# Kernel tuning notes

Hardware: AMD Instinct MI355X
Metric: run time of the kernel (lower is better)

The kernel has to match this reference:

```python
import jax, jax.numpy as jnp
import numpy as np

HEADS = 8
DIM_HEAD = 64
EPS = 1e-5  # PyTorch InstanceNorm default eps


def _instance_norm_lastdim(t):
    # PyTorch InstanceNorm1d on (b*h, n, d) with affine=False normalizes over
    # the last (spatial) axis d per (sample, token), biased variance.
    mu = jnp.mean(t, axis=-1, keepdims=True)
    var = jnp.mean(jnp.square(t - mu), axis=-1, keepdims=True)
    return (t - mu) / jnp.sqrt(var + EPS)


def setup_inputs() -> dict:
    key = jax.random.key(0)
    k1, k2, k3, k4, k5 = jax.random.split(key, 5)
    b, n1, n2, dim = 4, 8192, 8192, 256
    inner = HEADS * DIM_HEAD  # 512
    return {
        "x": jax.random.normal(k1, (b, n1, dim), jnp.float32),
        "z": jax.random.normal(k2, (b, n2, dim), jnp.float32),
        "Wq": jax.random.normal(k3, (dim, inner), jnp.float32) * 0.02,
        "Wkv": jax.random.normal(k4, (dim, 2 * inner), jnp.float32) * 0.02,
        "Wout": jax.random.normal(k5, (inner, dim), jnp.float32) * 0.02,
        "bout": jnp.zeros((dim,), jnp.float32),
    }


def reference(x, z, Wq, Wkv, Wout, bout):
    b, n1, _ = x.shape
    n2 = z.shape[1]
    h, d = HEADS, DIM_HEAD

    q = x @ Wq                     # [b, n1, h*d]
    kv = z @ Wkv                   # [b, n2, 2*h*d]
    k, v = jnp.split(kv, 2, axis=-1)

    q = q.reshape(b, n1, h, d).transpose(0, 2, 1, 3)  # b h n1 d
    k = k.reshape(b, n2, h, d).transpose(0, 2, 1, 3)  # b h n2 d
    v = v.reshape(b, n2, h, d).transpose(0, 2, 1, 3)  # b h n2 d

    # galerkin: normalize k and v
    k = _instance_norm_lastdim(k)
    v = _instance_norm_lastdim(v)

    # linear-attention kernel trick: (k^T v) then q @ dots, scaled by 1/n2
    dots = jnp.einsum('bhnd,bhne->bhde', k, v)          # [b, h, d, d]
    out = jnp.einsum('bhnd,bhde->bhne', q, dots) / n2   # [b, h, n1, d]

    out = out.transpose(0, 2, 1, 3).reshape(b, n1, h * d)
    return out @ Wout + bout
```

## Files before the change

### kernel.cpp

```cpp
#include <hip/hip_runtime.h>
#include <cstddef>

#define NB    4
#define NTOK  8192
#define DIMX  256
#define NH    8
#define HD    64
#define INNER 512
#define SPLIT 16
#define EPS   1e-5f

typedef __attribute__((ext_vector_type(8))) short short8;
typedef __attribute__((ext_vector_type(4))) float f32x4;

__device__ __forceinline__ unsigned short f2bf(float f) {
  union { float f; unsigned u; } v; v.f = f;
  unsigned r = v.u + 0x7fffu + ((v.u >> 16) & 1u);
  return (unsigned short)(r >> 16);
}

__global__ __launch_bounds__(256) void k_pre(
    const float* __restrict__ z, unsigned short* __restrict__ zb,
    const float* __restrict__ Wkv, unsigned short* __restrict__ wkvT)
{
  __shared__ unsigned short t[64][68];
  if (blockIdx.x < 2048) {
    const size_t i = ((size_t)blockIdx.x * 256 + threadIdx.x) * 16;
    float4 a0 = *(const float4*)(z + i);
    float4 a1 = *(const float4*)(z + i + 4);
    float4 a2 = *(const float4*)(z + i + 8);
    float4 a3 = *(const float4*)(z + i + 12);
    short8 p0, p1;
    p0[0] = (short)f2bf(a0.x); p0[1] = (short)f2bf(a0.y);
    p0[2] = (short)f2bf(a0.z); p0[3] = (short)f2bf(a0.w);
    p0[4] = (short)f2bf(a1.x); p0[5] = (short)f2bf(a1.y);
    p0[6] = (short)f2bf(a1.z); p0[7] = (short)f2bf(a1.w);
    p1[0] = (short)f2bf(a2.x); p1[1] = (short)f2bf(a2.y);
    p1[2] = (short)f2bf(a2.z); p1[3] = (short)f2bf(a2.w);
    p1[4] = (short)f2bf(a3.x); p1[5] = (short)f2bf(a3.y);
    p1[6] = (short)f2bf(a3.z); p1[7] = (short)f2bf(a3.w);
    *(short8*)(zb + i) = p0;
    *(short8*)(zb + i + 8) = p1;
  } else {
    const int tid = threadIdx.x;
    const int bb = blockIdx.x - 2048;
    const int r0 = (bb & 3) * 64;
    const int c0 = (bb >> 2) * 64;
    const int r = tid >> 2;
    const int c4 = (tid & 3) * 16;
#pragma unroll
    for (int j = 0; j < 4; ++j) {
      float4 v = *(const float4*)(Wkv + (size_t)(r0 + r) * (2 * INNER) + c0 + c4 + j * 4);
      t[r][c4 + j * 4 + 0] = f2bf(v.x);
      t[r][c4 + j * 4 + 1] = f2bf(v.y);
      t[r][c4 + j * 4 + 2] = f2bf(v.z);
      t[r][c4 + j * 4 + 3] = f2bf(v.w);
    }
    __syncthreads();
    const int cc = tid >> 2;
    const int rr4 = (tid & 3) * 16;
    short8 o0, o1;
#pragma unroll
    for (int i = 0; i < 8; ++i) o0[i] = (short)t[rr4 + i][cc];
#pragma unroll
    for (int i = 0; i < 8; ++i) o1[i] = (short)t[rr4 + 8 + i][cc];
    unsigned short* dst = wkvT + (size_t)(c0 + cc) * DIMX + r0 + rr4;
    *(short8*)(dst) = o0;
    *(short8*)(dst + 8) = o1;
  }
}

__global__ __launch_bounds__(256) void k_dots_mfma(
    const unsigned short* __restrict__ zb, const unsigned short* __restrict__ wkvT,
    float* __restrict__ partial)
{
  const int tid  = threadIdx.x;
  const int lane = tid & 63;
  const int w    = tid >> 6;
  const int l15  = lane & 15;
  const int lg   = lane >> 4;

  const int bid = blockIdx.x;
  const int s = bid & (SPLIT - 1);
  const int h = (bid >> 4) & (NH - 1);
  const int b = bid >> 7;

  __shared__ unsigned short zs[32][268];
  __shared__ unsigned short kv2[128][36];
  __shared__ float sum1[4][32];
  __shared__ float sum2[4][32];

  short8 awf[2][8];
#pragma unroll
  for (int mf = 0; mf < 2; ++mf) {
    const int dim = w * 32 + mf * 16 + l15;
    const int gd = (dim < HD) ? (h * HD + dim) : (INNER + h * HD + (dim - HD));
    const unsigned short* base = wkvT + (size_t)gd * DIMX + lg * 8;
#pragma unroll
    for (int kk = 0; kk < 8; ++kk)
      awf[mf][kk] = *(const short8*)(base + kk * 32);
  }

  f32x4 dacc[4];
#pragma unroll
  for (int nf = 0; nf < 4; ++nf) dacc[nf] = (f32x4){0.f, 0.f, 0.f, 0.f};

  const int zr = tid >> 3;
  const int zc = (tid & 7) * 32;
  const unsigned short* zbase = zb + ((size_t)b * NTOK + s * 512 + zr) * DIMX + zc;

  {
    short8 pre[4];
#pragma unroll
    for (int j = 0; j < 4; ++j) pre[j] = *(const short8*)(zbase + j * 8);
#pragma unroll
    for (int j = 0; j < 4; ++j) *(short8*)&zs[zr][zc + j * 8] = pre[j];
  }
  __syncthreads();

  for (int tile = 0; tile < 16; ++tile) {
    short8 pre[4];
    if (tile < 15) {
      const unsigned short* src = zbase + (size_t)(tile + 1) * 32 * DIMX;
#pragma unroll
      for (int j = 0; j < 4; ++j) pre[j] = *(const short8*)(src + j * 8);
    }

    f32x4 acc[2][2];
#pragma unroll
    for (int mf = 0; mf < 2; ++mf)
#pragma unroll
      for (int nf = 0; nf < 2; ++nf) acc[mf][nf] = (f32x4){0.f, 0.f, 0.f, 0.f};

#pragma unroll
    for (int kk = 0; kk < 8; ++kk) {
      short8 bfr[2];
#pragma unroll
      for (int nf = 0; nf < 2; ++nf)
        bfr[nf] = *(const short8*)&zs[nf * 16 + l15][kk * 32 + lg * 8];
#pragma unroll
      for (int mf = 0; mf < 2; ++mf)
#pragma unroll
        for (int nf = 0; nf < 2; ++nf)
          acc[mf][nf] = __builtin_amdgcn_mfma_f32_16x16x32_bf16(
              awf[mf][kk], bfr[nf], acc[mf][nf], 0, 0, 0);
    }

    float s1[2], s2[2];
#pragma unroll
    for (int nf = 0; nf < 2; ++nf) {
      float a = 0.f, q = 0.f;
#pragma unroll
      for (int mf = 0; mf < 2; ++mf)
#pragma unroll
        for (int r = 0; r < 4; ++r) {
          float v = acc[mf][nf][r];
          a += v; q += v * v;
        }
      a += __shfl_xor(a, 16); a += __shfl_xor(a, 32);
      q += __shfl_xor(q, 16); q += __shfl_xor(q, 32);
      s1[nf] = a; s2[nf] = q;
    }
    if (lg == 0) {
#pragma unroll
      for (int nf = 0; nf < 2; ++nf) {
        sum1[w][nf * 16 + l15] = s1[nf];
        sum2[w][nf * 16 + l15] = s2[nf];
      }
    }
    __syncthreads();

    if (tile < 15) {
#pragma unroll
      for (int j = 0; j < 4; ++j) *(short8*)&zs[zr][zc + j * 8] = pre[j];
    }

    if (w < 2) {
      const int p = w ^ 1;
      float mu[2];
#pragma unroll
      for (int nf = 0; nf < 2; ++nf)
        mu[nf] = (s1[nf] + sum1[p][nf * 16 + l15]) * (1.f / 64.f);
#pragma unroll
      for (int mf = 0; mf < 2; ++mf)
#pragma unroll
        for (int nf = 0; nf < 2; ++nf)
#pragma unroll
          for (int r = 0; r < 4; ++r)
            kv2[w * 32 + mf * 16 + lg * 4 + r][nf * 16 + l15] =
                f2bf(acc[mf][nf][r] - mu[nf]);
    } else {
      const int p = w ^ 1;
      float sc[2], ms[2];
#pragma unroll
      for (int nf = 0; nf < 2; ++nf) {
        const int tok = nf * 16 + l15;
        const float t1v = s1[nf] + sum1[p][tok];
        const float t2v = s2[nf] + sum2[p][tok];
        const float muv = t1v * (1.f / 64.f);
        const float rv = rsqrtf(t2v * (1.f / 64.f) - muv * muv + EPS);
        const float t1k = sum1[0][tok] + sum1[1][tok];
        const float t2k = sum2[0][tok] + sum2[1][tok];
        const float muk = t1k * (1.f / 64.f);
        const float rk = rsqrtf(t2k * (1.f / 64.f) - muk * muk + EPS);
        sc[nf] = rk * rv;
        ms[nf] = muv * sc[nf];
      }
#pragma unroll
      for (int mf = 0; mf < 2; ++mf)
#pragma unroll
        for (int nf = 0; nf < 2; ++nf)
#pragma unroll
          for (int r = 0; r < 4; ++r)
            kv2[(w - 2) * 32 + 64 + mf * 16 + lg * 4 + r][nf * 16 + l15] =
                f2bf(fmaf(acc[mf][nf][r], sc[nf], -ms[nf]));
    }
    __syncthreads();

    {
      short8 a2 = *(const short8*)&kv2[w * 16 + l15][lg * 8];
#pragma unroll
      for (int nf = 0; nf < 4; ++nf) {
        short8 b2 = *(const short8*)&kv2[64 + nf * 16 + l15][lg * 8];
        dacc[nf] = __builtin_amdgcn_mfma_f32_16x16x32_bf16(a2, b2, dacc[nf], 0, 0, 0);
      }
    }
  }

  float* pb = partial + ((size_t)((b * NH + h) * SPLIT + s)) * 4096;
#pragma unroll
  for (int nf = 0; nf < 4; ++nf)
#pragma unroll
    for (int r = 0; r < 4; ++r)
      pb[(w * 16 + lg * 4 + r) * 64 + nf * 16 + l15] = dacc[nf][r];
}

__global__ __launch_bounds__(256) void k_bdwout2(
    const float* __restrict__ partial, const float* __restrict__ Wout,
    float* __restrict__ tmp)
{
  const int bid = blockIdx.x;
  const int b = bid >> 7;
  const int r4 = (bid & 127) * 4;
  const int h = r4 >> 6;
  const int c = threadIdx.x;

  __shared__ float drow[4][64];
  {
    const int rr = c >> 6;
    const int j = c & 63;
    const float* p = partial + (size_t)(b * NH + h) * SPLIT * 4096
                   + ((r4 & 63) + rr) * 64 + j;
    float s = 0.f;
#pragma unroll
    for (int i = 0; i < SPLIT; ++i) s += p[(size_t)i * 4096];
    drow[rr][j] = s * (1.f / (float)NTOK);
  }
  __syncthreads();

  float a0 = 0.f, a1 = 0.f, a2 = 0.f, a3 = 0.f;
#pragma unroll 8
  for (int j = 0; j < 64; ++j) {
    const float wv = Wout[(size_t)(h * 64 + j) * DIMX + c];
    a0 += drow[0][j] * wv;
    a1 += drow[1][j] * wv;
    a2 += drow[2][j] * wv;
    a3 += drow[3][j] * wv;
  }
  float* tb = tmp + ((size_t)b * INNER + r4) * DIMX + c;
  tb[0] = a0; tb[DIMX] = a1; tb[2 * DIMX] = a2; tb[3 * DIMX] = a3;
}

__global__ __launch_bounds__(256) void k_weff(
    const float* __restrict__ Wq, const float* __restrict__ tmp,
    unsigned short* __restrict__ weffT)
{
  const int bid = blockIdx.x;
  const int b = bid >> 7;
  const int r2 = (bid & 127) * 2;
  const int c = threadIdx.x;
  const float* tb = tmp + (size_t)b * INNER * DIMX + c;
  float a0 = 0.f, a1 = 0.f;
#pragma unroll 16
  for (int k = 0; k < INNER; ++k) {
    const float t = tb[(size_t)k * DIMX];
    a0 += Wq[(size_t)(r2 + 0) * INNER + k] * t;
    a1 += Wq[(size_t)(r2 + 1) * INNER + k] * t;
  }
  unsigned short* wb = weffT + ((size_t)b * DIMX + c) * DIMX + r2;
  wb[0] = f2bf(a0); wb[1] = f2bf(a1);
}

__global__ __launch_bounds__(256) void k_out_mfma(
    const float* __restrict__ x, const unsigned short* __restrict__ weffT,
    const float* __restrict__ bout, float* __restrict__ out)
{
  const int tid  = threadIdx.x;
  const int lane = tid & 63;
  const int w    = tid >> 6;
  const int l15  = lane & 15;
  const int lg   = lane >> 4;

  const int bid = blockIdx.x;
  const int mt = bid & 127;
  const int ct = (bid >> 7) & 1;
  const int b  = bid >> 8;
  const int tok0 = mt * 64;
  const int col0 = ct * 128;

  __shared__ unsigned short wsl[2][128 * 36];

  short8 afr[8];
  {
    const float* xr = x + ((size_t)b * NTOK + tok0 + w * 16 + l15) * DIMX + lg * 8;
#pragma unroll
    for (int kk = 0; kk < 8; ++kk) {
      float4 xa = *(const float4*)(xr + kk * 32);
      float4 xb = *(const float4*)(xr + kk * 32 + 4);
      short8 a;
      a[0] = (short)f2bf(xa.x); a[1] = (short)f2bf(xa.y);
      a[2] = (short)f2bf(xa.z); a[3] = (short)f2bf(xa.w);
      a[4] = (short)f2bf(xb.x); a[5] = (short)f2bf(xb.y);
      a[6] = (short)f2bf(xb.z); a[7] = (short)f2bf(xb.w);
      afr[kk] = a;
    }
  }

  f32x4 acc[8];
#pragma unroll
  for (int nf = 0; nf < 8; ++nf) acc[nf] = (f32x4){0.f, 0.f, 0.f, 0.f};

  const unsigned short* wb = weffT + (size_t)b * DIMX * DIMX
                           + (size_t)(col0 + (tid >> 1)) * DIMX + (tid & 1) * 16;
  const int c36 = (tid >> 1) * 36 + (tid & 1) * 16;

  *(short8*)&wsl[0][c36]     = *(const short8*)(wb);
  *(short8*)&wsl[0][c36 + 8] = *(const short8*)(wb + 8);
  __syncthreads();

  for (int kk = 0; kk < 8; ++kk) {
    short8 g0, g1;
    if (kk < 7) {
      g0 = *(const short8*)(wb + (kk + 1) * 32);
      g1 = *(const short8*)(wb + (kk + 1) * 32 + 8);
    }
#pragma unroll
    for (int nf = 0; nf < 8; ++nf) {
      short8 b2 = *(const short8*)&wsl[kk & 1][(nf * 16 + l15) * 36 + lg * 8];
      acc[nf] = __builtin_amdgcn_mfma_f32_16x16x32_bf16(afr[kk], b2, acc[nf], 0, 0, 0);
    }
    if (kk < 7) {
      *(short8*)&wsl[(kk + 1) & 1][c36]     = g0;
      *(short8*)&wsl[(kk + 1) & 1][c36 + 8] = g1;
    }
    __syncthreads();
  }

#pragma unroll
  for (int nf = 0; nf < 8; ++nf) {
    const float bias = bout[col0 + nf * 16 + l15];
#pragma unroll
    for (int r = 0; r < 4; ++r) {
      const int row = tok0 + w * 16 + lg * 4 + r;
      out[((size_t)b * NTOK + row) * DIMX + col0 + nf * 16 + l15] = acc[nf][r] + bias;
    }
  }
}

extern "C" void kernel_launch(void* const* d_in, const int* in_sizes, int n_in,
                              void* d_out, int out_size, void* d_ws, size_t ws_size,
                              hipStream_t stream) {
  const float* x    = (const float*)d_in[0];
  const float* z    = (const float*)d_in[1];
  const float* Wq   = (const float*)d_in[2];
  const float* Wkv  = (const float*)d_in[3];
  const float* Wout = (const float*)d_in[4];
  const float* bout = (const float*)d_in[5];
  float* out = (float*)d_out;

  float* ws  = (float*)d_ws;
  float* tmp = ws;
  unsigned short* wkvT  = (unsigned short*)(tmp + (size_t)NB * INNER * DIMX);
  unsigned short* weffT = wkvT + (size_t)(2 * INNER) * DIMX;

  unsigned short* zbf = (unsigned short*)d_out;
  float* partial = (float*)((char*)d_out + ((size_t)16 << 20));

  k_pre<<<2112, 256, 0, stream>>>(z, zbf, Wkv, wkvT);
  k_dots_mfma<<<NB * NH * SPLIT, 256, 0, stream>>>(zbf, wkvT, partial);
  k_bdwout2<<<NB * 128, 256, 0, stream>>>(partial, Wout, tmp);
  k_weff<<<NB * 128, 256, 0, stream>>>(Wq, tmp, weffT);
  k_out_mfma<<<NB * 256, 256, 0, stream>>>(x, weffT, bout, out);
}
```

Measured before the change: 92.15 us.

## Process two heads per block in dots kernel with wave-local norms and double buffering

The K/V projection-and-dots kernel now handles two heads per block, with each wave computing one full 64-wide K or V slice. Instance-norm statistics therefore reduce inside a single wave, with no shared-memory exchange between waves. The z tile and the kv2 tile are double-buffered, so each tile needs one barrier instead of two. Each z tile is reused across two heads, and the token split doubles to keep the block count unchanged. The cost is more registers (launch bounds of 256 threads with a minimum of 2 blocks), more LDS, and twice as many partial sums to reduce. Separately, k_weff now computes 8 Wq rows per block over 4x fewer blocks, which gives more reuse of tmp per block but less parallelism.

```diff
diff --git a/kernel.cpp b/kernel.cpp
--- a/kernel.cpp
+++ b/kernel.cpp
@@ -7,7 +7,7 @@
 #define NH    8
 #define HD    64
 #define INNER 512
-#define SPLIT 16
+#define SPLIT 32
 #define EPS   1e-5f
 
 typedef __attribute__((ext_vector_type(8))) short short8;
@@ -70,65 +70,69 @@
   }
 }
 
-__global__ __launch_bounds__(256) void k_dots_mfma(
+__global__ __launch_bounds__(256, 2) void k_dots_mfma(
     const unsigned short* __restrict__ zb, const unsigned short* __restrict__ wkvT,
     float* __restrict__ partial)
 {
   const int tid  = threadIdx.x;
   const int lane = tid & 63;
   const int w    = tid >> 6;
+  const int hh   = w >> 1;
+  const int side = w & 1;
   const int l15  = lane & 15;
   const int lg   = lane >> 4;
 
   const int bid = blockIdx.x;
-  const int s = bid & (SPLIT - 1);
-  const int h = (bid >> 4) & (NH - 1);
-  const int b = bid >> 7;
-
-  __shared__ unsigned short zs[32][268];
-  __shared__ unsigned short kv2[128][36];
-  __shared__ float sum1[4][32];
-  __shared__ float sum2[4][32];
-
-  short8 awf[2][8];
-#pragma unroll
-  for (int mf = 0; mf < 2; ++mf) {
-    const int dim = w * 32 + mf * 16 + l15;
-    const int gd = (dim < HD) ? (h * HD + dim) : (INNER + h * HD + (dim - HD));
+  const int s  = bid & (SPLIT - 1);
+  const int hp = (bid >> 5) & 3;
+  const int b  = bid >> 7;
+  const int h  = hp * 2 + hh;
+
+  __shared__ unsigned short zs[2][32][268];
+  __shared__ unsigned short kv2[2][256][36];
+
+  short8 awf[4][8];
+#pragma unroll
+  for (int mf = 0; mf < 4; ++mf) {
+    const int dim = mf * 16 + l15;
+    const int gd = (side == 0) ? (h * HD + dim) : (INNER + h * HD + dim);
     const unsigned short* base = wkvT + (size_t)gd * DIMX + lg * 8;
 #pragma unroll
     for (int kk = 0; kk < 8; ++kk)
       awf[mf][kk] = *(const short8*)(base + kk * 32);
   }
 
-  f32x4 dacc[4];
-#pragma unroll
-  for (int nf = 0; nf < 4; ++nf) dacc[nf] = (f32x4){0.f, 0.f, 0.f, 0.f};
+  f32x4 dacc[2][4];
+#pragma unroll
+  for (int mfr = 0; mfr < 2; ++mfr)
+#pragma unroll
+    for (int nfc = 0; nfc < 4; ++nfc) dacc[mfr][nfc] = (f32x4){0.f, 0.f, 0.f, 0.f};
 
   const int zr = tid >> 3;
   const int zc = (tid & 7) * 32;
-  const unsigned short* zbase = zb + ((size_t)b * NTOK + s * 512 + zr) * DIMX + zc;
+  const unsigned short* zbase = zb + ((size_t)b * NTOK + s * 256 + zr) * DIMX + zc;
 
   {
     short8 pre[4];
 #pragma unroll
     for (int j = 0; j < 4; ++j) pre[j] = *(const short8*)(zbase + j * 8);
 #pragma unroll
-    for (int j = 0; j < 4; ++j) *(short8*)&zs[zr][zc + j * 8] = pre[j];
+    for (int j = 0; j < 4; ++j) *(short8*)&zs[0][zr][zc + j * 8] = pre[j];
   }
   __syncthreads();
 
-  for (int tile = 0; tile < 16; ++tile) {
+  int cur = 0;
+  for (int tile = 0; tile < 8; ++tile) {
     short8 pre[4];
-    if (tile < 15) {
+    if (tile < 7) {
       const unsigned short* src = zbase + (size_t)(tile + 1) * 32 * DIMX;
 #pragma unroll
       for (int j = 0; j < 4; ++j) pre[j] = *(const short8*)(src + j * 8);
     }
 
-    f32x4 acc[2][2];
-#pragma unroll
-    for (int mf = 0; mf < 2; ++mf)
+    f32x4 acc[4][2];
+#pragma unroll
+    for (int mf = 0; mf < 4; ++mf)
 #pragma unroll
       for (int nf = 0; nf < 2; ++nf) acc[mf][nf] = (f32x4){0.f, 0.f, 0.f, 0.f};
 
@@ -137,21 +141,21 @@
       short8 bfr[2];
 #pragma unroll
       for (int nf = 0; nf < 2; ++nf)
-        bfr[nf] = *(const short8*)&zs[nf * 16 + l15][kk * 32 + lg * 8];
-#pragma unroll
-      for (int mf = 0; mf < 2; ++mf)
+        bfr[nf] = *(const short8*)&zs[cur][nf * 16 + l15][kk * 32 + lg * 8];
+#pragma unroll
+      for (int mf = 0; mf < 4; ++mf)
 #pragma unroll
         for (int nf = 0; nf < 2; ++nf)
           acc[mf][nf] = __builtin_amdgcn_mfma_f32_16x16x32_bf16(
               awf[mf][kk], bfr[nf], acc[mf][nf], 0, 0, 0);
     }
 
-    float s1[2], s2[2];
+    float mu[2], rs[2];
 #pragma unroll
     for (int nf = 0; nf < 2; ++nf) {
       float a = 0.f, q = 0.f;
 #pragma unroll
-      for (int mf = 0; mf < 2; ++mf)
+      for (int mf = 0; mf < 4; ++mf)
 #pragma unroll
         for (int r = 0; r < 4; ++r) {
           float v = acc[mf][nf][r];
@@ -159,80 +163,54 @@
         }
       a += __shfl_xor(a, 16); a += __shfl_xor(a, 32);
       q += __shfl_xor(q, 16); q += __shfl_xor(q, 32);
-      s1[nf] = a; s2[nf] = q;
-    }
-    if (lg == 0) {
-#pragma unroll
-      for (int nf = 0; nf < 2; ++nf) {
-        sum1[w][nf * 16 + l15] = s1[nf];
-        sum2[w][nf * 16 + l15] = s2[nf];
-      }
+      const float m = a * (1.f / 64.f);
+      mu[nf] = m;
+      rs[nf] = rsqrtf(q * (1.f / 64.f) - m * m + EPS);
+    }
+
+#pragma unroll
+    for (int mf = 0; mf < 4; ++mf)
+#pragma unroll
+      for (int nf = 0; nf < 2; ++nf)
+#pragma unroll
+        for (int r = 0; r < 4; ++r)
+          kv2[cur][hh * 128 + side * 64 + mf * 16 + lg * 4 + r][nf * 16 + l15] =
+              f2bf((acc[mf][nf][r] - mu[nf]) * rs[nf]);
+
+    if (tile < 7) {
+#pragma unroll
+      for (int j = 0; j < 4; ++j) *(short8*)&zs[cur ^ 1][zr][zc + j * 8] = pre[j];
     }
     __syncthreads();
 
-    if (tile < 15) {
-#pragma unroll
-      for (int j = 0; j < 4; ++j) *(short8*)&zs[zr][zc + j * 8] = pre[j];
-    }
-
-    if (w < 2) {
-      const int p = w ^ 1;
-      float mu[2];
-#pragma unroll
-      for (int nf = 0; nf < 2; ++nf)
-        mu[nf] = (s1[nf] + sum1[p][nf * 16 + l15]) * (1.f / 64.f);
-#pragma unroll
-      for (int mf = 0; mf < 2; ++mf)
-#pragma unroll
-        for (int nf = 0; nf < 2; ++nf)
-#pragma unroll
-          for (int r = 0; r < 4; ++r)
-            kv2[w * 32 + mf * 16 + lg * 4 + r][nf * 16 + l15] =
-                f2bf(acc[mf][nf][r] - mu[nf]);
-    } else {
-      const int p = w ^ 1;
-      float sc[2], ms[2];
-#pragma unroll
-      for (int nf = 0; nf < 2; ++nf) {
-        const int tok = nf * 16 + l15;
-        const float t1v = s1[nf] + sum1[p][tok];
-        const float t2v = s2[nf] + sum2[p][tok];
-        const float muv = t1v * (1.f / 64.f);
-        const float rv = rsqrtf(t2v * (1.f / 64.f) - muv * muv + EPS);
-        const float t1k = sum1[0][tok] + sum1[1][tok];
-        const float t2k = sum2[0][tok] + sum2[1][tok];
-        const float muk = t1k * (1.f / 64.f);
-        const float rk = rsqrtf(t2k * (1.f / 64.f) - muk * muk + EPS);
-        sc[nf] = rk * rv;
-        ms[nf] = muv * sc[nf];
-      }
-#pragma unroll
-      for (int mf = 0; mf < 2; ++mf)
-#pragma unroll
-        for (int nf = 0; nf < 2; ++nf)
-#pragma unroll
-          for (int r = 0; r < 4; ++r)
-            kv2[(w - 2) * 32 + 64 + mf * 16 + lg * 4 + r][nf * 16 + l15] =
-                f2bf(fmaf(acc[mf][nf][r], sc[nf], -ms[nf]));
-    }
-    __syncthreads();
-
     {
-      short8 a2 = *(const short8*)&kv2[w * 16 + l15][lg * 8];
-#pragma unroll
-      for (int nf = 0; nf < 4; ++nf) {
-        short8 b2 = *(const short8*)&kv2[64 + nf * 16 + l15][lg * 8];
-        dacc[nf] = __builtin_amdgcn_mfma_f32_16x16x32_bf16(a2, b2, dacc[nf], 0, 0, 0);
-      }
-    }
+      const int kvb = hh * 128;
+      short8 a2[2], b2[4];
+#pragma unroll
+      for (int mfr = 0; mfr < 2; ++mfr)
+        a2[mfr] = *(const short8*)&kv2[cur][kvb + side * 32 + mfr * 16 + l15][lg * 8];
+#pragma unroll
+      for (int nfc = 0; nfc < 4; ++nfc)
+        b2[nfc] = *(const short8*)&kv2[cur][kvb + 64 + nfc * 16 + l15][lg * 8];
+#pragma unroll
+      for (int mfr = 0; mfr < 2; ++mfr)
+#pragma unroll
+        for (int nfc = 0; nfc < 4; ++nfc)
+          dacc[mfr][nfc] = __builtin_amdgcn_mfma_f32_16x16x32_bf16(
+              a2[mfr], b2[nfc], dacc[mfr][nfc], 0, 0, 0);
+    }
+    cur ^= 1;
   }
 
   float* pb = partial + ((size_t)((b * NH + h) * SPLIT + s)) * 4096;
 #pragma unroll
-  for (int nf = 0; nf < 4; ++nf)
-#pragma unroll
-    for (int r = 0; r < 4; ++r)
-      pb[(w * 16 + lg * 4 + r) * 64 + nf * 16 + l15] = dacc[nf][r];
+  for (int mfr = 0; mfr < 2; ++mfr)
+#pragma unroll
+    for (int nfc = 0; nfc < 4; ++nfc)
+#pragma unroll
+      for (int r = 0; r < 4; ++r)
+        pb[(side * 32 + mfr * 16 + lg * 4 + r) * 64 + nfc * 16 + l15] =
+            dacc[mfr][nfc][r];
 }
 
 __global__ __launch_bounds__(256) void k_bdwout2(
@@ -276,19 +254,23 @@
     unsigned short* __restrict__ weffT)
 {
   const int bid = blockIdx.x;
-  const int b = bid >> 7;
-  const int r2 = (bid & 127) * 2;
+  const int b = bid >> 5;
+  const int r8 = (bid & 31) * 8;
   const int c = threadIdx.x;
   const float* tb = tmp + (size_t)b * INNER * DIMX + c;
-  float a0 = 0.f, a1 = 0.f;
-#pragma unroll 16
+  float a[8];
+#pragma unroll
+  for (int i = 0; i < 8; ++i) a[i] = 0.f;
+#pragma unroll 8
   for (int k = 0; k < INNER; ++k) {
     const float t = tb[(size_t)k * DIMX];
-    a0 += Wq[(size_t)(r2 + 0) * INNER + k] * t;
-    a1 += Wq[(size_t)(r2 + 1) * INNER + k] * t;
-  }
-  unsigned short* wb = weffT + ((size_t)b * DIMX + c) * DIMX + r2;
-  wb[0] = f2bf(a0); wb[1] = f2bf(a1);
+#pragma unroll
+    for (int i = 0; i < 8; ++i)
+      a[i] += Wq[(size_t)(r8 + i) * INNER + k] * t;
+  }
+  unsigned short* wb = weffT + ((size_t)b * DIMX + c) * DIMX + r8;
+#pragma unroll
+  for (int i = 0; i < 8; ++i) wb[i] = f2bf(a[i]);
 }
 
 __global__ __launch_bounds__(256) void k_out_mfma(
@@ -387,8 +369,8 @@
   float* partial = (float*)((char*)d_out + ((size_t)16 << 20));
 
   k_pre<<<2112, 256, 0, stream>>>(z, zbf, Wkv, wkvT);
-  k_dots_mfma<<<NB * NH * SPLIT, 256, 0, stream>>>(zbf, wkvT, partial);
+  k_dots_mfma<<<NB * (NH / 2) * SPLIT, 256, 0, stream>>>(zbf, wkvT, partial);
   k_bdwout2<<<NB * 128, 256, 0, stream>>>(partial, Wout, tmp);
-  k_weff<<<NB * 128, 256, 0, stream>>>(Wq, tmp, weffT);
+  k_weff<<<NB * 32, 256, 0, stream>>>(Wq, tmp, weffT);
   k_out_mfma<<<NB * 256, 256, 0, stream>>>(x, weffT, bout, out);
 }
```

Measured after the change: 115.0 us. +24.8%, slower.
